# Kernel tuning notes

Measured on AMD Instinct MI355X. Metric: run time of the kernel, lower is better.

Reference implementation:

```python
import jax, jax.numpy as jnp
import numpy as np

N_NODES = 50000
N_RAND_EDGES = 800000
NEG_SLOPE = 0.2


def gat_conv(h, src, dst, W, attn_l, attn_r, bias, res_W=None, act=False):
    # DGL GATConv semantics: fc -> per-node attn halves -> per-edge leaky_relu
    # logits -> segment softmax over destination -> weighted scatter-sum.
    N = h.shape[0]
    H, D = attn_l.shape
    feat = (h @ W).reshape(N, H, D)                      # (N,H,D)
    el = (feat * attn_l[None]).sum(-1)                   # (N,H)
    er = (feat * attn_r[None]).sum(-1)                   # (N,H)
    e = jax.nn.leaky_relu(el[src] + er[dst], NEG_SLOPE)  # (E,H)
    emax = jax.ops.segment_max(e, dst, num_segments=N)   # (N,H)
    ee = jnp.exp(e - emax[dst])                          # (E,H)
    denom = jax.ops.segment_sum(ee, dst, num_segments=N)
    alpha = ee / denom[dst]                              # (E,H)
    msg = feat[src] * alpha[:, :, None]                  # (E,H,D) dominant traffic
    rst = jax.ops.segment_sum(msg, dst, num_segments=N)  # (N,H,D)
    if res_W is not None:
        rst = rst + (h @ res_W).reshape(N, H, D)
    rst = rst + bias.reshape(1, H, D)
    if act:
        rst = jax.nn.relu(rst)
    return rst


def setup_inputs() -> dict:
    key = jax.random.key(0)
    ks = jax.random.split(key, 20)
    x = jax.random.normal(ks[0], (N_NODES, 64), dtype=jnp.float32)
    src_r = jax.random.randint(ks[1], (N_RAND_EDGES,), 0, N_NODES, dtype=jnp.int32)
    dst_r = jax.random.randint(ks[2], (N_RAND_EDGES,), 0, N_NODES, dtype=jnp.int32)
    loops = jnp.arange(N_NODES, dtype=jnp.int32)
    src = jnp.concatenate([src_r, loops])   # self-loops: no zero in-degree
    dst = jnp.concatenate([dst_r, loops])
    s = 0.1
    p = lambda k, shp: jax.random.normal(k, shp, dtype=jnp.float32) * s
    return {
        "x": x, "src": src, "dst": dst,
        # layer 1: in=64 -> hid=32, heads=4, relu, no residual
        "W1": p(ks[3], (64, 128)), "al1": p(ks[4], (4, 32)), "ar1": p(ks[5], (4, 32)),
        "b1": jnp.zeros((128,), jnp.float32),
        # layer 2: in=128 -> hid=32, heads=4, relu, residual
        "W2": p(ks[6], (128, 128)), "al2": p(ks[7], (4, 32)), "ar2": p(ks[8], (4, 32)),
        "b2": jnp.zeros((128,), jnp.float32), "resW2": p(ks[9], (128, 128)),
        # layer 3: in=128 -> out=1, heads=6, no activation, residual
        "W3": p(ks[10], (128, 6)), "al3": p(ks[11], (6, 1)), "ar3": p(ks[12], (6, 1)),
        "b3": jnp.zeros((6,), jnp.float32), "resW3": p(ks[13], (128, 6)),
    }


def reference(x, src, dst, W1, al1, ar1, b1, W2, al2, ar2, b2, resW2,
              W3, al3, ar3, b3, resW3):
    h = gat_conv(x, src, dst, W1, al1, ar1, b1, None, act=True)
    h = h.reshape(h.shape[0], -1)                        # flatten heads
    h = gat_conv(h, src, dst, W2, al2, ar2, b2, resW2, act=True)
    h = h.reshape(h.shape[0], -1)
    h = gat_conv(h, src, dst, W3, al3, ar3, b3, resW3, act=False)
    return h.mean(axis=1)                                # mean over heads -> (N, out)
```

## Files before the change

### kernel.cpp

```cpp
#include <hip/hip_runtime.h>
#include <hip/hip_fp16.h>

#define NEG 0.2f
#define BUCKET_SHIFT 7
#define CAP 3200
#define PCHUNK 4096

template <int K>
__global__ __launch_bounds__(256) void gemm_el_k(const float* __restrict__ A,
                                                 const float* __restrict__ W,
                                                 const float* __restrict__ al,
                                                 const float* __restrict__ ar,
                                                 __half* __restrict__ feat_h,
                                                 float* __restrict__ el,
                                                 float* __restrict__ er, int N) {
    __shared__ float As[64 * K];
    const int c = threadIdx.x & 31;
    const int rg = threadIdx.x >> 5;
    const int row0 = blockIdx.x << 6;
    const int K4 = K >> 2;

    const float4* Av = (const float4*)A;
    float4* AsV = (float4*)As;
    for (int idx = threadIdx.x; idx < 16 * K; idx += 256) {
        int rr = idx / K4, kk4 = idx - rr * K4;
        int row = row0 + rr;
        float4 v = make_float4(0.f, 0.f, 0.f, 0.f);
        if (row < N) v = Av[(size_t)row * K4 + kk4];
        AsV[rr * K4 + kk4] = v;
    }
    __syncthreads();

    const float4* Wv = (const float4*)W;
    float4 acc[8];
#pragma unroll
    for (int i = 0; i < 8; i++) acc[i] = make_float4(0.f, 0.f, 0.f, 0.f);

    for (int k4 = 0; k4 < K4; k4++) {
        float4 a[8];
#pragma unroll
        for (int i = 0; i < 8; i++) a[i] = AsV[(rg * 8 + i) * K4 + k4];
#pragma unroll
        for (int kk = 0; kk < 4; kk++) {
            float4 w = Wv[((k4 << 2) + kk) * 32 + c];
#pragma unroll
            for (int i = 0; i < 8; i++) {
                float av = kk == 0 ? a[i].x : kk == 1 ? a[i].y : kk == 2 ? a[i].z : a[i].w;
                acc[i].x += av * w.x;
                acc[i].y += av * w.y;
                acc[i].z += av * w.z;
                acc[i].w += av * w.w;
            }
        }
    }

    __half2* Fh2 = (__half2*)feat_h;
#pragma unroll
    for (int i = 0; i < 8; i++) {
        int row = row0 + rg * 8 + i;
        if (row < N) {
            size_t o = ((size_t)row << 6) + (c << 1);
            Fh2[o] = __floats2half2_rn(acc[i].x, acc[i].y);
            Fh2[o + 1] = __floats2half2_rn(acc[i].z, acc[i].w);
        }
    }

    float4 alv = ((const float4*)al)[c];
    float4 arv = ((const float4*)ar)[c];
    float pel[8], per_[8];
#pragma unroll
    for (int i = 0; i < 8; i++) {
        pel[i] = acc[i].x * alv.x + acc[i].y * alv.y + acc[i].z * alv.z + acc[i].w * alv.w;
        per_[i] = acc[i].x * arv.x + acc[i].y * arv.y + acc[i].z * arv.z + acc[i].w * arv.w;
    }
#pragma unroll
    for (int m = 1; m < 8; m <<= 1) {
#pragma unroll
        for (int i = 0; i < 8; i++) {
            pel[i] += __shfl_xor(pel[i], m);
            per_[i] += __shfl_xor(per_[i], m);
        }
    }
    if ((c & 7) == 0) {
        int h = c >> 3;
#pragma unroll
        for (int i = 0; i < 8; i++) {
            int row = row0 + rg * 8 + i;
            if (row < N) {
                el[(row << 2) + h] = pel[i];
                er[(row << 2) + h] = per_[i];
            }
        }
    }
}

template <int K>
__global__ __launch_bounds__(256) void gemm_res_k(const float* __restrict__ A,
                                                  const float* __restrict__ W,
                                                  const float* __restrict__ bias,
                                                  float* __restrict__ C, int N) {
    __shared__ float As[64 * K];
    const int c = threadIdx.x & 31;
    const int rg = threadIdx.x >> 5;
    const int row0 = blockIdx.x << 6;
    const int K4 = K >> 2;

    const float4* Av = (const float4*)A;
    float4* AsV = (float4*)As;
    for (int idx = threadIdx.x; idx < 16 * K; idx += 256) {
        int rr = idx / K4, kk4 = idx - rr * K4;
        int row = row0 + rr;
        float4 v = make_float4(0.f, 0.f, 0.f, 0.f);
        if (row < N) v = Av[(size_t)row * K4 + kk4];
        AsV[rr * K4 + kk4] = v;
    }
    __syncthreads();

    const float4* Wv = (const float4*)W;
    float4 acc[8];
#pragma unroll
    for (int i = 0; i < 8; i++) acc[i] = make_float4(0.f, 0.f, 0.f, 0.f);

    for (int k4 = 0; k4 < K4; k4++) {
        float4 a[8];
#pragma unroll
        for (int i = 0; i < 8; i++) a[i] = AsV[(rg * 8 + i) * K4 + k4];
#pragma unroll
        for (int kk = 0; kk < 4; kk++) {
            float4 w = Wv[((k4 << 2) + kk) * 32 + c];
#pragma unroll
            for (int i = 0; i < 8; i++) {
                float av = kk == 0 ? a[i].x : kk == 1 ? a[i].y : kk == 2 ? a[i].z : a[i].w;
                acc[i].x += av * w.x;
                acc[i].y += av * w.y;
                acc[i].z += av * w.z;
                acc[i].w += av * w.w;
            }
        }
    }

    float4* Cv = (float4*)C;
    float4 bv = ((const float4*)bias)[c];
#pragma unroll
    for (int i = 0; i < 8; i++) {
        int row = row0 + rg * 8 + i;
        if (row < N) {
            size_t o = ((size_t)row << 5) + c;
            float4 cur = Cv[o];
            float4 v;
            v.x = fmaxf(cur.x + acc[i].x + bv.x, 0.f);
            v.y = fmaxf(cur.y + acc[i].y + bv.y, 0.f);
            v.z = fmaxf(cur.z + acc[i].z + bv.z, 0.f);
            v.w = fmaxf(cur.w + acc[i].w + bv.w, 0.f);
            Cv[o] = v;
        }
    }
}

__global__ __launch_bounds__(256) void partition_k(const int* __restrict__ src,
                                                   const int* __restrict__ dst,
                                                   int* __restrict__ cursor,
                                                   unsigned* __restrict__ part,
                                                   int E, int NB) {
    __shared__ unsigned stash[PCHUNK];
    __shared__ int hist[512];
    __shared__ int base[512];
    const int tid = threadIdx.x;
    const int e0 = blockIdx.x * PCHUNK;

    for (int i = tid; i < NB; i += 256) hist[i] = 0;
    __syncthreads();

    for (int i = tid; i < PCHUNK; i += 256) {
        int e = e0 + i;
        unsigned pk = 0xFFFFFFFFu;
        if (e < E) {
            int d = dst[e];
            pk = ((unsigned)d << 16) | (unsigned)src[e];
            atomicAdd(&hist[d >> BUCKET_SHIFT], 1);
        }
        stash[i] = pk;
    }
    __syncthreads();

    for (int i = tid; i < NB; i += 256) {
        int hcnt = hist[i];
        base[i] = hcnt ? atomicAdd(&cursor[i], hcnt) : 0;
        hist[i] = 0;
    }
    __syncthreads();

    for (int i = tid; i < PCHUNK; i += 256) {
        unsigned pk = stash[i];
        if (pk != 0xFFFFFFFFu) {
            int b = pk >> (16 + BUCKET_SHIFT);
            int r = base[b] + atomicAdd(&hist[b], 1);
            if (r < CAP) part[(size_t)b * CAP + r] = pk;
        }
    }
}

__global__ __launch_bounds__(256) void bucket_csr_k(const int* __restrict__ cursor,
                                                    const unsigned* __restrict__ part,
                                                    int* __restrict__ csr_src,
                                                    int* __restrict__ row_beg,
                                                    int* __restrict__ row_end,
                                                    int N) {
    __shared__ int cnt[128], sc[128], ex[128], cur[128];
    __shared__ int lcsr[CAP];
    const int b = blockIdx.x;
    const int tid = threadIdx.x;
    int m = cursor[b];
    m = m < CAP ? m : CAP;
    if (tid < 128) cnt[tid] = 0;
    __syncthreads();

    const unsigned* pp = part + (size_t)b * CAP;
    for (int i = tid; i < m; i += 256) atomicAdd(&cnt[(pp[i] >> 16) & 127], 1);
    __syncthreads();

    if (tid < 128) sc[tid] = cnt[tid];
    __syncthreads();
    for (int off = 1; off < 128; off <<= 1) {
        int t = (tid < 128 && tid >= off) ? sc[tid - off] : 0;
        __syncthreads();
        if (tid < 128) sc[tid] += t;
        __syncthreads();
    }
    if (tid < 128) {
        ex[tid] = sc[tid] - cnt[tid];
        cur[tid] = 0;
    }
    __syncthreads();

    for (int i = tid; i < m; i += 256) {
        unsigned pk = pp[i];
        int dlo = (pk >> 16) & 127;
        int r = atomicAdd(&cur[dlo], 1);
        lcsr[ex[dlo] + r] = (int)(pk & 0xFFFFu);
    }
    __syncthreads();

    const int gbase = b * CAP;
    for (int i = tid; i < m; i += 256) csr_src[gbase + i] = lcsr[i];
    int n = (b << BUCKET_SHIFT) + tid;
    if (tid < 128 && n < N) {
        row_beg[n] = gbase + ex[tid];
        row_end[n] = gbase + sc[tid];
    }
}

template <bool BR>
__global__ __launch_bounds__(256) void pull2_k(const int* __restrict__ row_beg,
                                               const int* __restrict__ row_end,
                                               const int* __restrict__ csr_src,
                                               const float* __restrict__ el,
                                               const float* __restrict__ er,
                                               const __half* __restrict__ feat_h,
                                               const float* __restrict__ bias,
                                               float* __restrict__ outp, int N) {
    int n = (blockIdx.x << 2) + (threadIdx.x >> 6);
    if (n >= N) return;
    unsigned l = threadIdx.x & 63;
    unsigned h = l >> 4;
    float erd = er[((unsigned)n << 2) + h];
    const __half2* feat2 = (const __half2*)feat_h;
    int beg = __builtin_amdgcn_readfirstlane(row_beg[n]);
    int end = __builtin_amdgcn_readfirstlane(row_end[n]);
    float ax = 0.f, ay = 0.f, den = 0.f;
    int p = beg;
    for (; p + 4 <= end; p += 4) {
        int s0 = csr_src[p], s1 = csr_src[p + 1];
        int s2 = csr_src[p + 2], s3 = csr_src[p + 3];
        float e0 = el[((unsigned)s0 << 2) + h];
        float e1 = el[((unsigned)s1 << 2) + h];
        float e2 = el[((unsigned)s2 << 2) + h];
        float e3 = el[((unsigned)s3 << 2) + h];
        __half2 g0 = feat2[((unsigned)s0 << 6) + l];
        __half2 g1 = feat2[((unsigned)s1 << 6) + l];
        __half2 g2 = feat2[((unsigned)s2 << 6) + l];
        __half2 g3 = feat2[((unsigned)s3 << 6) + l];
        float x0 = e0 + erd, x1 = e1 + erd, x2 = e2 + erd, x3 = e3 + erd;
        x0 = fmaxf(x0, NEG * x0);
        x1 = fmaxf(x1, NEG * x1);
        x2 = fmaxf(x2, NEG * x2);
        x3 = fmaxf(x3, NEG * x3);
        float w0 = __expf(x0), w1 = __expf(x1), w2 = __expf(x2), w3 = __expf(x3);
        float2 f0 = __half22float2(g0), f1 = __half22float2(g1);
        float2 f2 = __half22float2(g2), f3 = __half22float2(g3);
        den += (w0 + w1) + (w2 + w3);
        ax = fmaf(w0, f0.x, ax);
        ay = fmaf(w0, f0.y, ay);
        ax = fmaf(w1, f1.x, ax);
        ay = fmaf(w1, f1.y, ay);
        ax = fmaf(w2, f2.x, ax);
        ay = fmaf(w2, f2.y, ay);
        ax = fmaf(w3, f3.x, ax);
        ay = fmaf(w3, f3.y, ay);
    }
    for (; p < end; p++) {
        int s0 = csr_src[p];
        float e0 = el[((unsigned)s0 << 2) + h];
        __half2 g0 = feat2[((unsigned)s0 << 6) + l];
        float x0 = e0 + erd;
        x0 = fmaxf(x0, NEG * x0);
        float w0 = __expf(x0);
        float2 f0 = __half22float2(g0);
        den += w0;
        ax = fmaf(w0, f0.x, ax);
        ay = fmaf(w0, f0.y, ay);
    }
    float inv = 1.f / den;
    float2 v;
    v.x = ax * inv;
    v.y = ay * inv;
    if (BR) {
        float2 b = ((const float2*)bias)[l];
        v.x = fmaxf(v.x + b.x, 0.f);
        v.y = fmaxf(v.y + b.y, 0.f);
    }
    ((float2*)outp)[((size_t)n << 6) + l] = v;
}

__global__ __launch_bounds__(256) void feat3res_k(const float* __restrict__ h3,
                                                  const float* __restrict__ W3,
                                                  const float* __restrict__ resW3,
                                                  const float* __restrict__ b3,
                                                  float* __restrict__ feat3,
                                                  float* __restrict__ res3, int N) {
    int n = blockIdx.x * blockDim.x + threadIdx.x;
    if (n >= N) return;
    const float4* a = (const float4*)(h3 + ((size_t)n << 7));
    float f[6], r[6];
#pragma unroll
    for (int h = 0; h < 6; h++) {
        f[h] = 0.f;
        r[h] = b3[h];
    }
    for (int k4 = 0; k4 < 32; k4++) {
        float4 v = a[k4];
        int k = k4 << 2;
#pragma unroll
        for (int h = 0; h < 6; h++) {
            f[h] += v.x * W3[(k + 0) * 6 + h] + v.y * W3[(k + 1) * 6 + h] +
                    v.z * W3[(k + 2) * 6 + h] + v.w * W3[(k + 3) * 6 + h];
            r[h] += v.x * resW3[(k + 0) * 6 + h] + v.y * resW3[(k + 1) * 6 + h] +
                    v.z * resW3[(k + 2) * 6 + h] + v.w * resW3[(k + 3) * 6 + h];
        }
    }
#pragma unroll
    for (int h = 0; h < 6; h++) {
        feat3[n * 6 + h] = f[h];
        res3[n * 6 + h] = r[h];
    }
}

__global__ __launch_bounds__(256) void pull6_k(const int* __restrict__ row_beg,
                                               const int* __restrict__ row_end,
                                               const int* __restrict__ csr_src,
                                               const float* __restrict__ feat3,
                                               const float* __restrict__ al3,
                                               const float* __restrict__ ar3,
                                               const float* __restrict__ res3,
                                               float* __restrict__ rst3, int N) {
    int idx = blockIdx.x * blockDim.x + threadIdx.x;
    if (idx >= N * 6) return;
    int n = idx / 6, h = idx - n * 6;
    float a3 = al3[h], r3 = ar3[h];
    float fdr = feat3[idx] * r3;
    int beg = row_beg[n], end = row_end[n];
    float acc = 0.f, den = 0.f;
    int p = beg;
    for (; p + 2 <= end; p += 2) {
        int s0 = csr_src[p], s1 = csr_src[p + 1];
        float f0 = feat3[(unsigned)s0 * 6 + h];
        float f1 = feat3[(unsigned)s1 * 6 + h];
        float x0 = fmaf(f0, a3, fdr);
        float x1 = fmaf(f1, a3, fdr);
        x0 = fmaxf(x0, NEG * x0);
        x1 = fmaxf(x1, NEG * x1);
        float w0 = __expf(x0), w1 = __expf(x1);
        den += w0 + w1;
        acc = fmaf(w0, f0, acc);
        acc = fmaf(w1, f1, acc);
    }
    if (p < end) {
        int s0 = csr_src[p];
        float f0 = feat3[(unsigned)s0 * 6 + h];
        float x0 = fmaf(f0, a3, fdr);
        x0 = fmaxf(x0, NEG * x0);
        float w0 = __expf(x0);
        den += w0;
        acc = fmaf(w0, f0, acc);
    }
    rst3[idx] = acc / den + res3[idx];
}

__global__ __launch_bounds__(256) void final_k(const float* __restrict__ rst3,
                                               float* __restrict__ out, int N) {
    int n = blockIdx.x * blockDim.x + threadIdx.x;
    if (n >= N) return;
    const float2* r2 = (const float2*)(rst3 + n * 6);
    float2 a = r2[0], b = r2[1], c = r2[2];
    out[n] = (a.x + a.y + b.x + b.y + c.x + c.y) * (1.f / 6.f);
}

extern "C" void kernel_launch(void* const* d_in, const int* in_sizes, int n_in,
                              void* d_out, int out_size, void* d_ws, size_t ws_size,
                              hipStream_t stream) {
    const float* x = (const float*)d_in[0];
    const int* src = (const int*)d_in[1];
    const int* dst = (const int*)d_in[2];
    const float* W1 = (const float*)d_in[3];
    const float* al1 = (const float*)d_in[4];
    const float* ar1 = (const float*)d_in[5];
    const float* b1 = (const float*)d_in[6];
    const float* W2 = (const float*)d_in[7];
    const float* al2 = (const float*)d_in[8];
    const float* ar2 = (const float*)d_in[9];
    const float* b2 = (const float*)d_in[10];
    const float* resW2 = (const float*)d_in[11];
    const float* W3 = (const float*)d_in[12];
    const float* al3 = (const float*)d_in[13];
    const float* ar3 = (const float*)d_in[14];
    const float* b3 = (const float*)d_in[15];
    const float* resW3 = (const float*)d_in[16];
    float* out = (float*)d_out;

    const int N = in_sizes[0] / 64;
    const int E = in_sizes[1];
    const int NB = (N + 127) >> BUCKET_SHIFT;

    float* ws = (float*)d_ws;
    __half* feat_h = (__half*)ws;
    float* h2 = ws + (size_t)N * 64;
    float* h3 = h2 + (size_t)N * 128;
    float* el = h3 + (size_t)N * 128;
    float* er = el + (size_t)N * 4;
    float* feat3 = el;
    float* res3 = er + (size_t)N * 4;
    float* rst3 = res3 + (size_t)N * 6;
    int* ip = (int*)(rst3 + (size_t)N * 6);
    int* cursor = ip;
    int* row_beg = cursor + 512;
    int* row_end = row_beg + N;
    unsigned* part = (unsigned*)(row_end + N);
    int* csr_src = (int*)(part + (size_t)NB * CAP);

    const int gN = (N + 255) / 256;
    const int gN64 = (N + 63) / 64;
    const int gN6 = (N * 6 + 255) / 256;
    const int gNw = (N + 3) / 4;
    const int gP = (E + PCHUNK - 1) / PCHUNK;

    hipMemsetAsync(cursor, 0, sizeof(int) * 512, stream);
    partition_k<<<gP, 256, 0, stream>>>(src, dst, cursor, part, E, NB);
    bucket_csr_k<<<NB, 256, 0, stream>>>(cursor, part, csr_src, row_beg, row_end, N);

    gemm_el_k<64><<<gN64, 256, 0, stream>>>(x, W1, al1, ar1, feat_h, el, er, N);
    pull2_k<true><<<gNw, 256, 0, stream>>>(row_beg, row_end, csr_src, el, er,
                                           feat_h, b1, h2, N);

    gemm_el_k<128><<<gN64, 256, 0, stream>>>(h2, W2, al2, ar2, feat_h, el, er, N);
    pull2_k<false><<<gNw, 256, 0, stream>>>(row_beg, row_end, csr_src, el, er,
                                            feat_h, nullptr, h3, N);
    gemm_res_k<128><<<gN64, 256, 0, stream>>>(h2, resW2, b2, h3, N);

    feat3res_k<<<gN, 256, 0, stream>>>(h3, W3, resW3, b3, feat3, res3, N);
    pull6_k<<<gN6, 256, 0, stream>>>(row_beg, row_end, csr_src, feat3, al3, ar3,
                                     res3, rst3, N);
    final_k<<<gN, 256, 0, stream>>>(rst3, out, N);
}
```

Baseline: 302.8 us.

## Use fp16 MFMA for layer-2 GEMMs and fuse residual with layer-3 projection

Adds a kernel that converts W2 and resW2 into fp16 MFMA fragment layout. The layer-2 feature GEMM and the residual GEMM now use 16x16x32 f16 MFMA instead of scalar FMA. The residual GEMM is fused with bias, relu and the layer-3 W3/resW3 projections, which removes the separate feat3res kernel and the fp32 h3 round trip. Intermediate activations h2 and the aggregated result are now stored as fp16 to halve their traffic. The cost is reduced precision in the layer-2 inputs and weights, plus one extra small conversion launch.

```diff
diff --git a/kernel.cpp b/kernel.cpp
--- a/kernel.cpp
+++ b/kernel.cpp
@@ -5,6 +5,9 @@
 #define BUCKET_SHIFT 7
 #define CAP 3200
 #define PCHUNK 4096
+
+typedef _Float16 h8 __attribute__((ext_vector_type(8)));
+typedef float f4v __attribute__((ext_vector_type(4)));
 
 template <int K>
 __global__ __launch_bounds__(256) void gemm_el_k(const float* __restrict__ A,
@@ -94,65 +97,196 @@
     }
 }
 
-template <int K>
-__global__ __launch_bounds__(256) void gemm_res_k(const float* __restrict__ A,
-                                                  const float* __restrict__ W,
-                                                  const float* __restrict__ bias,
-                                                  float* __restrict__ C, int N) {
-    __shared__ float As[64 * K];
-    const int c = threadIdx.x & 31;
-    const int rg = threadIdx.x >> 5;
-    const int row0 = blockIdx.x << 6;
-    const int K4 = K >> 2;
-
-    const float4* Av = (const float4*)A;
-    float4* AsV = (float4*)As;
-    for (int idx = threadIdx.x; idx < 16 * K; idx += 256) {
-        int rr = idx / K4, kk4 = idx - rr * K4;
-        int row = row0 + rr;
+__global__ __launch_bounds__(256) void wconv_k(const float* __restrict__ W2,
+                                               const float* __restrict__ rW2,
+                                               float4* __restrict__ W2f,
+                                               float4* __restrict__ rW2f) {
+    int c = blockIdx.x * 256 + threadIdx.x;
+    int which = c >> 11;
+    int cc = c & 2047;
+    int kb = cc >> 9, rem = cc & 511, t = rem >> 6, lane = rem & 63;
+    int n = (t << 4) + (lane & 15);
+    int k0 = (kb << 5) + ((lane >> 4) << 3);
+    const float* S = which ? rW2 : W2;
+    h8 v;
+#pragma unroll
+    for (int i = 0; i < 8; i++) v[i] = (_Float16)S[(k0 + i) * 128 + n];
+    ((h8*)(which ? rW2f : W2f))[cc] = v;
+}
+
+#define MFMA_STAGE_AND_LOOP()                                                   \
+    const int tid = threadIdx.x;                                                \
+    const int row0 = blockIdx.x << 6;                                           \
+    for (int i = tid; i < 2048; i += 256) WsF[i] = Wf[i];                       \
+    const float4* Afv = (const float4*)A;                                       \
+    for (int idx = tid; idx < 1024; idx += 256) {                               \
+        int r = idx >> 4, kc = idx & 15;                                        \
+        float4 v = make_float4(0.f, 0.f, 0.f, 0.f);                             \
+        int row = row0 + r;                                                     \
+        if (row < N) v = Afv[(size_t)row * 16 + kc];                            \
+        int d = ((r >> 4) * 4 + (kc >> 2)) * 64 + (kc & 3) * 16 + (r & 15);     \
+        AsF[d] = v;                                                             \
+    }                                                                           \
+    __syncthreads();                                                            \
+    const int w = tid >> 6;                                                     \
+    const int lane = tid & 63;                                                  \
+    const h8* Ah = (const h8*)AsF;                                              \
+    const h8* Wh = (const h8*)WsF;                                              \
+    f4v acc[8];                                                                 \
+    _Pragma("unroll") for (int t = 0; t < 8; t++) acc[t] = (f4v){0.f, 0.f, 0.f, 0.f}; \
+    _Pragma("unroll") for (int kb = 0; kb < 4; kb++) {                          \
+        h8 af = Ah[(w * 4 + kb) * 64 + lane];                                   \
+        _Pragma("unroll") for (int t = 0; t < 8; t++) {                         \
+            h8 bf = Wh[(kb * 8 + t) * 64 + lane];                               \
+            acc[t] = __builtin_amdgcn_mfma_f32_16x16x32_f16(af, bf, acc[t], 0, 0, 0); \
+        }                                                                       \
+    }                                                                           \
+    const int c16 = lane & 15;                                                  \
+    const int rg = lane >> 4;
+
+__global__ __launch_bounds__(256) void mfma_el_k(const _Float16* __restrict__ A,
+                                                 const float4* __restrict__ Wf,
+                                                 const float* __restrict__ al,
+                                                 const float* __restrict__ ar,
+                                                 _Float16* __restrict__ feat,
+                                                 float* __restrict__ el,
+                                                 float* __restrict__ er, int N) {
+    __shared__ float4 WsF[2048];
+    __shared__ float4 AsF[1024];
+    MFMA_STAGE_AND_LOOP()
+
+    float alv[8], arv[8];
+#pragma unroll
+    for (int t = 0; t < 8; t++) {
+        alv[t] = al[(t << 4) + c16];
+        arv[t] = ar[(t << 4) + c16];
+    }
+    float pel[4][4], per_[4][4];
+#pragma unroll
+    for (int j = 0; j < 4; j++)
+#pragma unroll
+        for (int hh = 0; hh < 4; hh++) {
+            pel[j][hh] = acc[2 * hh][j] * alv[2 * hh] + acc[2 * hh + 1][j] * alv[2 * hh + 1];
+            per_[j][hh] = acc[2 * hh][j] * arv[2 * hh] + acc[2 * hh + 1][j] * arv[2 * hh + 1];
+        }
+#pragma unroll
+    for (int m = 1; m < 16; m <<= 1)
+#pragma unroll
+        for (int j = 0; j < 4; j++)
+#pragma unroll
+            for (int hh = 0; hh < 4; hh++) {
+                pel[j][hh] += __shfl_xor(pel[j][hh], m);
+                per_[j][hh] += __shfl_xor(per_[j][hh], m);
+            }
+    if (c16 == 0) {
+#pragma unroll
+        for (int j = 0; j < 4; j++) {
+            int row = row0 + (w << 4) + (rg << 2) + j;
+            if (row < N) {
+                ((float4*)el)[row] = make_float4(pel[j][0], pel[j][1], pel[j][2], pel[j][3]);
+                ((float4*)er)[row] = make_float4(per_[j][0], per_[j][1], per_[j][2], per_[j][3]);
+            }
+        }
+    }
+
+    _Float16* As2 = (_Float16*)AsF + (w << 11);
+#pragma unroll
+    for (int t = 0; t < 8; t++)
+#pragma unroll
+        for (int j = 0; j < 4; j++)
+            As2[((rg << 2) + j) * 128 + (t << 4) + c16] = (_Float16)acc[t][j];
+    __asm__ volatile("s_waitcnt lgkmcnt(0)" ::: "memory");
+    const float4* As2v = (const float4*)As2;
+    float4* featv = (float4*)feat;
+#pragma unroll
+    for (int ii = 0; ii < 4; ii++) {
+        int ch = ii * 64 + lane;
+        int row = row0 + (w << 4) + (ch >> 4);
+        if (row < N) featv[(size_t)row * 16 + (ch & 15)] = As2v[ch];
+    }
+}
+
+__global__ __launch_bounds__(256) void mfma_res_k(const _Float16* __restrict__ A,
+                                                  const float4* __restrict__ Wf,
+                                                  const _Float16* __restrict__ rsth,
+                                                  const float* __restrict__ b2,
+                                                  const float* __restrict__ W3,
+                                                  const float* __restrict__ resW3,
+                                                  const float* __restrict__ b3,
+                                                  float* __restrict__ feat3,
+                                                  float* __restrict__ res3, int N) {
+    __shared__ float4 WsF[2048];
+    __shared__ float4 AsF[1024];
+    MFMA_STAGE_AND_LOOP()
+
+    float4* As2v = (float4*)AsF + (w << 8);
+#pragma unroll
+    for (int ii = 0; ii < 4; ii++) {
+        int ch = ii * 64 + lane;
+        int row = row0 + (w << 4) + (ch >> 4);
         float4 v = make_float4(0.f, 0.f, 0.f, 0.f);
-        if (row < N) v = Av[(size_t)row * K4 + kk4];
-        AsV[rr * K4 + kk4] = v;
-    }
-    __syncthreads();
-
-    const float4* Wv = (const float4*)W;
-    float4 acc[8];
-#pragma unroll
-    for (int i = 0; i < 8; i++) acc[i] = make_float4(0.f, 0.f, 0.f, 0.f);
-
-    for (int k4 = 0; k4 < K4; k4++) {
-        float4 a[8];
-#pragma unroll
-        for (int i = 0; i < 8; i++) a[i] = AsV[(rg * 8 + i) * K4 + k4];
-#pragma unroll
-        for (int kk = 0; kk < 4; kk++) {
-            float4 w = Wv[((k4 << 2) + kk) * 32 + c];
-#pragma unroll
-            for (int i = 0; i < 8; i++) {
-                float av = kk == 0 ? a[i].x : kk == 1 ? a[i].y : kk == 2 ? a[i].z : a[i].w;
-                acc[i].x += av * w.x;
-                acc[i].y += av * w.y;
-                acc[i].z += av * w.z;
-                acc[i].w += av * w.w;
-            }
-        }
-    }
-
-    float4* Cv = (float4*)C;
-    float4 bv = ((const float4*)bias)[c];
-#pragma unroll
-    for (int i = 0; i < 8; i++) {
-        int row = row0 + rg * 8 + i;
-        if (row < N) {
-            size_t o = ((size_t)row << 5) + c;
-            float4 cur = Cv[o];
-            float4 v;
-            v.x = fmaxf(cur.x + acc[i].x + bv.x, 0.f);
-            v.y = fmaxf(cur.y + acc[i].y + bv.y, 0.f);
-            v.z = fmaxf(cur.z + acc[i].z + bv.z, 0.f);
-            v.w = fmaxf(cur.w + acc[i].w + bv.w, 0.f);
-            Cv[o] = v;
+        if (row < N) v = ((const float4*)rsth)[(size_t)row * 16 + (ch & 15)];
+        As2v[ch] = v;
+    }
+    __asm__ volatile("s_waitcnt lgkmcnt(0)" ::: "memory");
+    const _Float16* As2 = (const _Float16*)As2v;
+
+    float b2v[8];
+#pragma unroll
+    for (int t = 0; t < 8; t++) b2v[t] = b2[(t << 4) + c16];
+
+    float hv[8][4];
+#pragma unroll
+    for (int t = 0; t < 8; t++)
+#pragma unroll
+        for (int j = 0; j < 4; j++) {
+            float rv = (float)As2[((rg << 2) + j) * 128 + (t << 4) + c16];
+            hv[t][j] = fmaxf(acc[t][j] + rv + b2v[t], 0.f);
+        }
+
+    float f3[4][6], r3[4][6];
+#pragma unroll
+    for (int j = 0; j < 4; j++)
+#pragma unroll
+        for (int h = 0; h < 6; h++) {
+            f3[j][h] = 0.f;
+            r3[j][h] = 0.f;
+        }
+#pragma unroll
+    for (int t = 0; t < 8; t++) {
+        int col = (t << 4) + c16;
+        const float* w3p = W3 + col * 6;
+        const float* rwp = resW3 + col * 6;
+#pragma unroll
+        for (int h = 0; h < 6; h++) {
+            float w3 = w3p[h], rw = rwp[h];
+#pragma unroll
+            for (int j = 0; j < 4; j++) {
+                f3[j][h] = fmaf(hv[t][j], w3, f3[j][h]);
+                r3[j][h] = fmaf(hv[t][j], rw, r3[j][h]);
+            }
+        }
+    }
+#pragma unroll
+    for (int m = 1; m < 16; m <<= 1)
+#pragma unroll
+        for (int j = 0; j < 4; j++)
+#pragma unroll
+            for (int h = 0; h < 6; h++) {
+                f3[j][h] += __shfl_xor(f3[j][h], m);
+                r3[j][h] += __shfl_xor(r3[j][h], m);
+            }
+    if (c16 == 0) {
+#pragma unroll
+        for (int j = 0; j < 4; j++) {
+            int row = row0 + (w << 4) + (rg << 2) + j;
+            if (row < N) {
+#pragma unroll
+                for (int h = 0; h < 6; h++) {
+                    feat3[row * 6 + h] = f3[j][h];
+                    res3[row * 6 + h] = r3[j][h] + b3[h];
+                }
+            }
         }
     }
 }
@@ -258,7 +392,7 @@
                                                const float* __restrict__ er,
                                                const __half* __restrict__ feat_h,
                                                const float* __restrict__ bias,
-                                               float* __restrict__ outp, int N) {
+                                               __half* __restrict__ outp, int N) {
     int n = (blockIdx.x << 2) + (threadIdx.x >> 6);
     if (n >= N) return;
     unsigned l = threadIdx.x & 63;
@@ -311,48 +445,13 @@
         ay = fmaf(w0, f0.y, ay);
     }
     float inv = 1.f / den;
-    float2 v;
-    v.x = ax * inv;
-    v.y = ay * inv;
+    float vx = ax * inv, vy = ay * inv;
     if (BR) {
         float2 b = ((const float2*)bias)[l];
-        v.x = fmaxf(v.x + b.x, 0.f);
-        v.y = fmaxf(v.y + b.y, 0.f);
-    }
-    ((float2*)outp)[((size_t)n << 6) + l] = v;
-}
-
-__global__ __launch_bounds__(256) void feat3res_k(const float* __restrict__ h3,
-                                                  const float* __restrict__ W3,
-                                                  const float* __restrict__ resW3,
-                                                  const float* __restrict__ b3,
-                                                  float* __restrict__ feat3,
-                                                  float* __restrict__ res3, int N) {
-    int n = blockIdx.x * blockDim.x + threadIdx.x;
-    if (n >= N) return;
-    const float4* a = (const float4*)(h3 + ((size_t)n << 7));
-    float f[6], r[6];
-#pragma unroll
-    for (int h = 0; h < 6; h++) {
-        f[h] = 0.f;
-        r[h] = b3[h];
-    }
-    for (int k4 = 0; k4 < 32; k4++) {
-        float4 v = a[k4];
-        int k = k4 << 2;
-#pragma unroll
-        for (int h = 0; h < 6; h++) {
-            f[h] += v.x * W3[(k + 0) * 6 + h] + v.y * W3[(k + 1) * 6 + h] +
-                    v.z * W3[(k + 2) * 6 + h] + v.w * W3[(k + 3) * 6 + h];
-            r[h] += v.x * resW3[(k + 0) * 6 + h] + v.y * resW3[(k + 1) * 6 + h] +
-                    v.z * resW3[(k + 2) * 6 + h] + v.w * resW3[(k + 3) * 6 + h];
-        }
-    }
-#pragma unroll
-    for (int h = 0; h < 6; h++) {
-        feat3[n * 6 + h] = f[h];
-        res3[n * 6 + h] = r[h];
-    }
+        vx = fmaxf(vx + b.x, 0.f);
+        vy = fmaxf(vy + b.y, 0.f);
+    }
+    ((__half2*)outp)[((size_t)n << 6) + l] = __floats2half2_rn(vx, vy);
 }
 
 __global__ __launch_bounds__(256) void pull6_k(const int* __restrict__ row_beg,
@@ -432,15 +531,17 @@
     const int NB = (N + 127) >> BUCKET_SHIFT;
 
     float* ws = (float*)d_ws;
-    __half* feat_h = (__half*)ws;
-    float* h2 = ws + (size_t)N * 64;
-    float* h3 = h2 + (size_t)N * 128;
-    float* el = h3 + (size_t)N * 128;
+    __half* featA = (__half*)ws;
+    __half* h2h = (__half*)(ws + (size_t)N * 64);
+    __half* rsth = (__half*)(ws + (size_t)N * 128);
+    float* el = ws + (size_t)N * 192;
     float* er = el + (size_t)N * 4;
     float* feat3 = el;
-    float* res3 = er + (size_t)N * 4;
+    float* res3 = ws + (size_t)N * 200;
     float* rst3 = res3 + (size_t)N * 6;
-    int* ip = (int*)(rst3 + (size_t)N * 6);
+    float* W2f = rst3 + (size_t)N * 6;
+    float* rW2f = W2f + 8192;
+    int* ip = (int*)(rW2f + 8192);
     int* cursor = ip;
     int* row_beg = cursor + 512;
     int* row_end = row_beg + N;
@@ -454,19 +555,22 @@
     const int gP = (E + PCHUNK - 1) / PCHUNK;
 
     hipMemsetAsync(cursor, 0, sizeof(int) * 512, stream);
+    wconv_k<<<16, 256, 0, stream>>>(W2, resW2, (float4*)W2f, (float4*)rW2f);
     partition_k<<<gP, 256, 0, stream>>>(src, dst, cursor, part, E, NB);
     bucket_csr_k<<<NB, 256, 0, stream>>>(cursor, part, csr_src, row_beg, row_end, N);
 
-    gemm_el_k<64><<<gN64, 256, 0, stream>>>(x, W1, al1, ar1, feat_h, el, er, N);
+    gemm_el_k<64><<<gN64, 256, 0, stream>>>(x, W1, al1, ar1, featA, el, er, N);
     pull2_k<true><<<gNw, 256, 0, stream>>>(row_beg, row_end, csr_src, el, er,
-                                           feat_h, b1, h2, N);
-
-    gemm_el_k<128><<<gN64, 256, 0, stream>>>(h2, W2, al2, ar2, feat_h, el, er, N);
+                                           featA, b1, h2h, N);
+
+    mfma_el_k<<<gN64, 256, 0, stream>>>((const _Float16*)h2h, (const float4*)W2f,
+                                        al2, ar2, (_Float16*)featA, el, er, N);
     pull2_k<false><<<gNw, 256, 0, stream>>>(row_beg, row_end, csr_src, el, er,
-                                            feat_h, nullptr, h3, N);
-    gemm_res_k<128><<<gN64, 256, 0, stream>>>(h2, resW2, b2, h3, N);
-
-    feat3res_k<<<gN, 256, 0, stream>>>(h3, W3, resW3, b3, feat3, res3, N);
+                                            featA, nullptr, rsth, N);
+    mfma_res_k<<<gN64, 256, 0, stream>>>((const _Float16*)h2h, (const float4*)rW2f,
+                                         (const _Float16*)rsth, b2, W3, resW3, b3,
+                                         feat3, res3, N);
+
     pull6_k<<<gN6, 256, 0, stream>>>(row_beg, row_end, csr_src, feat3, al3, ar3,
                                      res3, rst3, N);
     final_k<<<gN, 256, 0, stream>>>(rst3, out, N);
```

Result: faster. 259.9 us (-14.2%).
